# Kernel tuning notes

Hardware: AMD Instinct MI355X
Metric: run time of the kernel (lower is better)

The kernel has to match this reference:

```python
import jax, jax.numpy as jnp
import numpy as np

TEMPERATURE = 0.5
NEG_FILL = -9e15


def setup_inputs() -> dict:
    key = jax.random.key(0)
    k1, k2 = jax.random.split(key)
    B, D = 8192, 128
    z1 = jax.random.normal(k1, (B, D), dtype=jnp.float32)
    z2 = jax.random.normal(k2, (B, D), dtype=jnp.float32)
    return {"z1": z1, "z2": z2}


def reference(z1, z2):
    B = z1.shape[0]
    N = 2 * B
    z = jnp.concatenate([z1, z2], axis=0)              # [N, D]
    sim = jnp.matmul(z, z.T) / TEMPERATURE             # [N, N]
    eye = jnp.eye(N, dtype=bool)
    sim = jnp.where(eye, NEG_FILL, sim)
    idx = jnp.arange(N)
    pos_idx = (idx + B) % N
    positives = sim[idx, pos_idx]                      # [N]
    loss = -positives + jax.scipy.special.logsumexp(sim, axis=1)
    return loss.mean()
```

## Files before the change

kernel.cpp:

```cpp
#include <hip/hip_runtime.h>
#include <stdint.h>


typedef __attribute__((ext_vector_type(8))) short s16x8;
typedef __attribute__((ext_vector_type(16))) float f32x16;

#define N_TOT   16384
#define NHALF   8192
#define DDIM    128
#define NQ      16
#define QW      (N_TOT / NQ)
#define BN      64
#define NT      (QW / BN)
#define BM      256
#define NRB     (N_TOT / BM)
#define CSH     128.0f
#define LN2     0.69314718055994530942f
#define BF_SCALE 1.6986436f

__device__ __forceinline__ unsigned short f2bf(float f) {
    union { float f; unsigned int u; } v; v.f = f;
    unsigned int u = v.u;
    unsigned int r = (u + 0x7FFFu + ((u >> 16) & 1u)) >> 16;
    return (unsigned short)r;
}

__device__ __forceinline__ void gload_lds16(const void* g, void* l) {
    __builtin_amdgcn_global_load_lds(
        (const __attribute__((address_space(1))) void*)g,
        (__attribute__((address_space(3))) void*)l, 16, 0, 0);
}

__global__ __launch_bounds__(256) void k_castpos(const float* __restrict__ z1,
                                                 const float* __restrict__ z2,
                                                 unsigned short* __restrict__ zb,
                                                 float* __restrict__ pos_part,
                                                 float* __restrict__ ws_acc) {
    __shared__ float red[4];
    int i = blockIdx.x * 256 + threadIdx.x;
    if (i == 0) { ws_acc[0] = 0.f; ((unsigned int*)ws_acc)[1] = 0u; }
    float4 a = ((const float4*)z1)[i];
    float4 b = ((const float4*)z2)[i];
    ushort4 oa, ob;
    oa.x = f2bf(a.x * BF_SCALE); oa.y = f2bf(a.y * BF_SCALE);
    oa.z = f2bf(a.z * BF_SCALE); oa.w = f2bf(a.w * BF_SCALE);
    ob.x = f2bf(b.x * BF_SCALE); ob.y = f2bf(b.y * BF_SCALE);
    ob.z = f2bf(b.z * BF_SCALE); ob.w = f2bf(b.w * BF_SCALE);
    ((ushort4*)zb)[i] = oa;
    ((ushort4*)(zb + (size_t)NHALF * DDIM))[i] = ob;
    float s = a.x * b.x + a.y * b.y + a.z * b.z + a.w * b.w;
    for (int o = 32; o; o >>= 1) s += __shfl_xor(s, o);
    int lane = threadIdx.x & 63, w = threadIdx.x >> 6;
    if (lane == 0) red[w] = s;
    __syncthreads();
    if (threadIdx.x == 0) pos_part[blockIdx.x] = red[0] + red[1] + red[2] + red[3];
}

#define MFMA_SUB(TBASE, SDX, O0, O1) do {                                     \
    const int c_  = (SDX) * 32 + l31;                                         \
    const int cx_ = c_ & 15;                                                  \
    const s16x8* tb_ = (TBASE) + c_ * 16;                                     \
    O0 = acc_init; O1 = acc_init;                                             \
    _Pragma("unroll")                                                         \
    for (int ks_ = 0; ks_ < 8; ++ks_) {                                       \
        s16x8 a_ = tb_[(ks_ * 2 + h) ^ cx_];                                  \
        O0 = __builtin_amdgcn_mfma_f32_32x32x16_bf16(a_, rf0[ks_], O0, 0,0,0);\
        O1 = __builtin_amdgcn_mfma_f32_32x32x16_bf16(a_, rf1[ks_], O1, 0,0,0);\
    } } while (0)

#define EXP_SUB(X0, X1, CB) do {                                              \
    if ((CB) == rowB) {                                                       \
        _Pragma("unroll")                                                     \
        for (int r2_ = 0; r2_ < 16; ++r2_) {                                  \
            int crow_ = (r2_ & 3) + 8 * (r2_ >> 2) + 4 * h;                   \
            if (crow_ == l31) X0[r2_] = -1e30f;                               \
        } }                                                                   \
    if ((CB) == rowB + 32) {                                                  \
        _Pragma("unroll")                                                     \
        for (int r2_ = 0; r2_ < 16; ++r2_) {                                  \
            int crow_ = (r2_ & 3) + 8 * (r2_ >> 2) + 4 * h;                   \
            if (crow_ == l31) X1[r2_] = -1e30f;                               \
        } }                                                                   \
    _Pragma("unroll")                                                         \
    for (int r2_ = 0; r2_ < 16; r2_ += 4) {                                   \
        sa[0] += __builtin_amdgcn_exp2f(X0[r2_ + 0]);                         \
        sa[1] += __builtin_amdgcn_exp2f(X0[r2_ + 1]);                         \
        sa[2] += __builtin_amdgcn_exp2f(X0[r2_ + 2]);                         \
        sa[3] += __builtin_amdgcn_exp2f(X0[r2_ + 3]);                         \
        sb[0] += __builtin_amdgcn_exp2f(X1[r2_ + 0]);                         \
        sb[1] += __builtin_amdgcn_exp2f(X1[r2_ + 1]);                         \
        sb[2] += __builtin_amdgcn_exp2f(X1[r2_ + 2]);                         \
        sb[3] += __builtin_amdgcn_exp2f(X1[r2_ + 3]);                         \
    } } while (0)

__global__ __launch_bounds__(256) void k_main(const unsigned short* __restrict__ zb,
                                              float* __restrict__ ps) {
    __shared__ s16x8 tile[2][BN * 16];

    const int tid  = threadIdx.x;
    const int lane = tid & 63;
    const int w    = tid >> 6;
    const int h    = lane >> 5;
    const int l31  = lane & 31;

    const int bid = blockIdx.x;
    const int q   = bid >> 6;
    const int rb  = bid & 63;
    const int rowB     = rb * BM + w * 64;
    const int colStart = q * QW;

    s16x8 rf0[8], rf1[8];
    {
        const s16x8* rp0 = (const s16x8*)(zb + (size_t)(rowB + l31) * DDIM);
        const s16x8* rp1 = (const s16x8*)(zb + (size_t)(rowB + 32 + l31) * DDIM);
        #pragma unroll
        for (int ks = 0; ks < 8; ++ks) { rf0[ks] = rp0[ks * 2 + h]; rf1[ks] = rp1[ks * 2 + h]; }
    }

    int soff[4];
    #pragma unroll
    for (int j = 0; j < 4; ++j) {
        int e = w * 4 + j;
        int col = e * 4 + (lane >> 4);
        int chunk = (lane & 15) ^ (col & 15);
        soff[j] = col * 256 + chunk * 16;
    }

    #pragma unroll
    for (int j = 0; j < 4; ++j)
        gload_lds16((const char*)zb + (size_t)colStart * 256 + soff[j],
                    (char*)(&tile[0][0]) + (w * 4 + j) * 1024);
    #pragma unroll
    for (int j = 0; j < 4; ++j)
        gload_lds16((const char*)zb + (size_t)(colStart + BN) * 256 + soff[j],
                    (char*)(&tile[1][0]) + (w * 4 + j) * 1024);

    const f32x16 acc_init = {-CSH, -CSH, -CSH, -CSH, -CSH, -CSH, -CSH, -CSH,
                             -CSH, -CSH, -CSH, -CSH, -CSH, -CSH, -CSH, -CSH};
    float sa[4] = {0.f, 0.f, 0.f, 0.f};
    float sb[4] = {0.f, 0.f, 0.f, 0.f};
    f32x16 A0, A1, B0, B1;
    int pcb;

    asm volatile("s_waitcnt vmcnt(4)" ::: "memory");
    __builtin_amdgcn_s_barrier();
    {
        const s16x8* tbase = &tile[0][0];
        MFMA_SUB(tbase, 0, A0, A1);
        MFMA_SUB(tbase, 1, B0, B1);
        EXP_SUB(A0, A1, colStart);
        pcb = colStart + 32;
    }
    __builtin_amdgcn_s_barrier();
    #pragma unroll
    for (int j = 0; j < 4; ++j)
        gload_lds16((const char*)zb + (size_t)(colStart + 2 * BN) * 256 + soff[j],
                    (char*)(&tile[0][0]) + (w * 4 + j) * 1024);

    for (int t = 1; t < NT; ++t) {
        if (t < NT - 1) asm volatile("s_waitcnt vmcnt(4)" ::: "memory");
        else            asm volatile("s_waitcnt vmcnt(0)" ::: "memory");
        __builtin_amdgcn_s_barrier();
        const s16x8* tbase = &tile[0][0] + (t & 1) * (BN * 16);
        const int cb0 = colStart + t * BN;
        MFMA_SUB(tbase, 0, A0, A1);
        EXP_SUB(B0, B1, pcb);
        MFMA_SUB(tbase, 1, B0, B1);
        EXP_SUB(A0, A1, cb0);
        pcb = cb0 + 32;
        __builtin_amdgcn_s_barrier();
        if (t + 2 < NT) {
            #pragma unroll
            for (int j = 0; j < 4; ++j)
                gload_lds16((const char*)zb + (size_t)(colStart + (t + 2) * BN) * 256 + soff[j],
                            (char*)(&tile[0][0]) + (t & 1) * 16384 + (w * 4 + j) * 1024);
        }
    }
    EXP_SUB(B0, B1, pcb);

    float sA = (sa[0] + sa[1]) + (sa[2] + sa[3]);
    float sB = (sb[0] + sb[1]) + (sb[2] + sb[3]);
    sA += __shfl_xor(sA, 32);
    sB += __shfl_xor(sB, 32);
    if (lane < 32) {
        ps[(size_t)q * N_TOT + rowB + l31]      = sA;
        ps[(size_t)q * N_TOT + rowB + 32 + l31] = sB;
    }
}

__global__ __launch_bounds__(256) void k_cf(const float* __restrict__ ps,
                                            const float* __restrict__ pos_part,
                                            float* __restrict__ ws_acc,
                                            float* __restrict__ out) {
    __shared__ float red[4];
    __shared__ int last;
    const int tid = threadIdx.x;
    const int base = blockIdx.x * 1024;
    float ls = 0.f;
    #pragma unroll
    for (int k = 0; k < 4; ++k) {
        int row = base + k * 256 + tid;
        float s = 0.f;
        #pragma unroll
        for (int qq = 0; qq < NQ; ++qq) s += ps[(size_t)qq * N_TOT + row];
        ls += LN2 * (CSH + log2f(s));
    }
    for (int o = 32; o; o >>= 1) ls += __shfl_xor(ls, o);
    int lane = tid & 63, wv = tid >> 6;
    if (lane == 0) red[wv] = ls;
    __syncthreads();
    if (tid == 0) {
        atomicAdd(&ws_acc[0], red[0] + red[1] + red[2] + red[3]);
        __threadfence();
        unsigned int old = atomicAdd(&((unsigned int*)ws_acc)[1], 1u);
        last = (old == 15u) ? 1 : 0;
    }
    __syncthreads();
    if (last) {
        float p = pos_part[tid] + pos_part[tid + 256] +
                  pos_part[tid + 512] + pos_part[tid + 768];
        for (int o = 32; o; o >>= 1) p += __shfl_xor(p, o);
        if (lane == 0) red[wv] = p;
        __syncthreads();
        if (tid == 0) {
            float lse_tot = atomicAdd(&ws_acc[0], 0.f);
            float pos_tot = red[0] + red[1] + red[2] + red[3];
            out[0] = (lse_tot - 4.0f * pos_tot) * (1.0f / (float)N_TOT);
        }
    }
}

extern "C" void kernel_launch(void* const* d_in, const int* in_sizes, int n_in,
                              void* d_out, int out_size, void* d_ws, size_t ws_size,
                              hipStream_t stream) {
    const float* z1 = (const float*)d_in[0];
    const float* z2 = (const float*)d_in[1];
    float* out = (float*)d_out;

    char* ws = (char*)d_ws;
    float* ps       = (float*)ws;
    float* ws_acc   = (float*)(ws + (1u << 20));
    float* pos_part = (float*)(ws + (1u << 20) + 1024);
    unsigned short* zb = (unsigned short*)(ws + (2u << 20));

    k_castpos<<<dim3(1024), dim3(256), 0, stream>>>(z1, z2, zb, pos_part, ws_acc);
    k_main<<<dim3(NRB * NQ), dim3(256), 0, stream>>>(zb, ps);
    k_cf<<<dim3(16), dim3(256), 0, stream>>>(ps, pos_part, ws_acc, out);
}
```

Baseline: 134.9 us.

## Switch similarity GEMM to int8 MFMA with polynomial exp2 on packed FMA

Quantizes the embeddings to int8 with a fixed scale instead of bf16 and computes the similarity tiles with 32x32x32 i8 MFMA, halving the bytes staged through LDS and the matrix-instruction count. The hardware exp2 is replaced by a bit-trick exponent split plus a cubic polynomial evaluated with packed v_pk_fma_f32, spreading the transcendental work onto FMA pipes. The software pipeline that overlapped one sub-tile's exp with the next MFMA is dropped in favor of a simpler sequential loop. It risks accuracy from int8 quantization, clamping and the approximate exp, and may lose MFMA/VALU overlap.

```diff
diff --git a/kernel.cpp b/kernel.cpp
--- a/kernel.cpp
+++ b/kernel.cpp
@@ -2,12 +2,12 @@
 #include <stdint.h>
 
 
-typedef __attribute__((ext_vector_type(8))) short s16x8;
-typedef __attribute__((ext_vector_type(16))) float f32x16;
+typedef __attribute__((ext_vector_type(4)))  int   i32x4;
+typedef __attribute__((ext_vector_type(16))) int   i32x16;
+typedef __attribute__((ext_vector_type(2)))  float f32x2;
 
 #define N_TOT   16384
 #define NHALF   8192
-#define DDIM    128
 #define NQ      16
 #define QW      (N_TOT / NQ)
 #define BN      64
@@ -16,14 +16,7 @@
 #define NRB     (N_TOT / BM)
 #define CSH     128.0f
 #define LN2     0.69314718055994530942f
-#define BF_SCALE 1.6986436f
-
-__device__ __forceinline__ unsigned short f2bf(float f) {
-    union { float f; unsigned int u; } v; v.f = f;
-    unsigned int u = v.u;
-    unsigned int r = (u + 0x7FFFu + ((u >> 16) & 1u)) >> 16;
-    return (unsigned short)r;
-}
+#define QS      27.178299f
 
 __device__ __forceinline__ void gload_lds16(const void* g, void* l) {
     __builtin_amdgcn_global_load_lds(
@@ -31,9 +24,24 @@
         (__attribute__((address_space(3))) void*)l, 16, 0, 0);
 }
 
+__device__ __forceinline__ f32x2 pk_fma(f32x2 a, f32x2 b, f32x2 c) {
+    f32x2 d;
+    asm("v_pk_fma_f32 %0, %1, %2, %3" : "=v"(d) : "v"(a), "v"(b), "v"(c));
+    return d;
+}
+
+__device__ __forceinline__ unsigned pack4(float4 f) {
+    int q0 = (int)rintf(fminf(fmaxf(f.x * QS, -127.f), 127.f));
+    int q1 = (int)rintf(fminf(fmaxf(f.y * QS, -127.f), 127.f));
+    int q2 = (int)rintf(fminf(fmaxf(f.z * QS, -127.f), 127.f));
+    int q3 = (int)rintf(fminf(fmaxf(f.w * QS, -127.f), 127.f));
+    return (unsigned)(q0 & 255) | ((unsigned)(q1 & 255) << 8) |
+           ((unsigned)(q2 & 255) << 16) | ((unsigned)q3 << 24);
+}
+
 __global__ __launch_bounds__(256) void k_castpos(const float* __restrict__ z1,
                                                  const float* __restrict__ z2,
-                                                 unsigned short* __restrict__ zb,
+                                                 unsigned* __restrict__ zb,
                                                  float* __restrict__ pos_part,
                                                  float* __restrict__ ws_acc) {
     __shared__ float red[4];
@@ -41,13 +49,8 @@
     if (i == 0) { ws_acc[0] = 0.f; ((unsigned int*)ws_acc)[1] = 0u; }
     float4 a = ((const float4*)z1)[i];
     float4 b = ((const float4*)z2)[i];
-    ushort4 oa, ob;
-    oa.x = f2bf(a.x * BF_SCALE); oa.y = f2bf(a.y * BF_SCALE);
-    oa.z = f2bf(a.z * BF_SCALE); oa.w = f2bf(a.w * BF_SCALE);
-    ob.x = f2bf(b.x * BF_SCALE); ob.y = f2bf(b.y * BF_SCALE);
-    ob.z = f2bf(b.z * BF_SCALE); ob.w = f2bf(b.w * BF_SCALE);
-    ((ushort4*)zb)[i] = oa;
-    ((ushort4*)(zb + (size_t)NHALF * DDIM))[i] = ob;
+    zb[i]          = pack4(a);
+    zb[i + 262144] = pack4(b);
     float s = a.x * b.x + a.y * b.y + a.z * b.z + a.w * b.w;
     for (int o = 32; o; o >>= 1) s += __shfl_xor(s, o);
     int lane = threadIdx.x & 63, w = threadIdx.x >> 6;
@@ -56,46 +59,55 @@
     if (threadIdx.x == 0) pos_part[blockIdx.x] = red[0] + red[1] + red[2] + red[3];
 }
 
-#define MFMA_SUB(TBASE, SDX, O0, O1) do {                                     \
-    const int c_  = (SDX) * 32 + l31;                                         \
-    const int cx_ = c_ & 15;                                                  \
-    const s16x8* tb_ = (TBASE) + c_ * 16;                                     \
-    O0 = acc_init; O1 = acc_init;                                             \
+#define MFMA_SUB(TB, SDX, O0, O1) do {                                        \
+    const int c_ = (SDX) * 32 + l31;                                          \
+    O0 = kZ16; O1 = kZ16;                                                     \
     _Pragma("unroll")                                                         \
-    for (int ks_ = 0; ks_ < 8; ++ks_) {                                       \
-        s16x8 a_ = tb_[(ks_ * 2 + h) ^ cx_];                                  \
-        O0 = __builtin_amdgcn_mfma_f32_32x32x16_bf16(a_, rf0[ks_], O0, 0,0,0);\
-        O1 = __builtin_amdgcn_mfma_f32_32x32x16_bf16(a_, rf1[ks_], O1, 0,0,0);\
+    for (int m_ = 0; m_ < 4; ++m_) {                                          \
+        i32x4 a_ = *(const i32x4*)((TB) + (m_ * 2 + h) * 1024 + c_ * 16);     \
+        O0 = __builtin_amdgcn_mfma_i32_32x32x32_i8(a_, rf0[m_], O0, 0, 0, 0); \
+        O1 = __builtin_amdgcn_mfma_i32_32x32x32_i8(a_, rf1[m_], O1, 0, 0, 0); \
     } } while (0)
+
+#define EXP_PAIR(AI0, AI1, S0, S1) do {                                       \
+    int i0_ = (AI0); i0_ = i0_ < 512 ? 512 : i0_;                             \
+    int i1_ = (AI1); i1_ = i1_ < 512 ? 512 : i1_;                             \
+    f32x2 af_; af_[0] = (float)i0_; af_[1] = (float)i1_;                      \
+    f32x2 T_ = pk_fma(af_, kD2, kMG);                                         \
+    f32x2 Nn_ = pk_fma(T_, kM1, kMG);                                         \
+    f32x2 F_ = pk_fma(af_, kD2, Nn_);                                         \
+    f32x2 P_ = pk_fma(F_, kC3, kC2);                                          \
+    P_ = pk_fma(F_, P_, kC1);                                                 \
+    P_ = pk_fma(F_, P_, kC0);                                                 \
+    unsigned n0_ = __float_as_uint(T_[0]) - 0x4B0000C0u;                      \
+    unsigned n1_ = __float_as_uint(T_[1]) - 0x4B0000C0u;                      \
+    S0 += __uint_as_float((n0_ << 23) + __float_as_uint(P_[0]));              \
+    S1 += __uint_as_float((n1_ << 23) + __float_as_uint(P_[1]));              \
+} while (0)
 
 #define EXP_SUB(X0, X1, CB) do {                                              \
     if ((CB) == rowB) {                                                       \
         _Pragma("unroll")                                                     \
         for (int r2_ = 0; r2_ < 16; ++r2_) {                                  \
             int crow_ = (r2_ & 3) + 8 * (r2_ >> 2) + 4 * h;                   \
-            if (crow_ == l31) X0[r2_] = -1e30f;                               \
+            if (crow_ == l31) X0[r2_] = -(1 << 30);                           \
         } }                                                                   \
     if ((CB) == rowB + 32) {                                                  \
         _Pragma("unroll")                                                     \
         for (int r2_ = 0; r2_ < 16; ++r2_) {                                  \
             int crow_ = (r2_ & 3) + 8 * (r2_ >> 2) + 4 * h;                   \
-            if (crow_ == l31) X1[r2_] = -1e30f;                               \
+            if (crow_ == l31) X1[r2_] = -(1 << 30);                           \
         } }                                                                   \
     _Pragma("unroll")                                                         \
-    for (int r2_ = 0; r2_ < 16; r2_ += 4) {                                   \
-        sa[0] += __builtin_amdgcn_exp2f(X0[r2_ + 0]);                         \
-        sa[1] += __builtin_amdgcn_exp2f(X0[r2_ + 1]);                         \
-        sa[2] += __builtin_amdgcn_exp2f(X0[r2_ + 2]);                         \
-        sa[3] += __builtin_amdgcn_exp2f(X0[r2_ + 3]);                         \
-        sb[0] += __builtin_amdgcn_exp2f(X1[r2_ + 0]);                         \
-        sb[1] += __builtin_amdgcn_exp2f(X1[r2_ + 1]);                         \
-        sb[2] += __builtin_amdgcn_exp2f(X1[r2_ + 2]);                         \
-        sb[3] += __builtin_amdgcn_exp2f(X1[r2_ + 3]);                         \
+    for (int p_ = 0; p_ < 8; ++p_) {                                          \
+        EXP_PAIR(X0[2 * p_], X0[2 * p_ + 1], sa[p_ & 3], sa[(p_ + 2) & 3]);   \
+        EXP_PAIR(X1[2 * p_], X1[2 * p_ + 1], sb[p_ & 3], sb[(p_ + 2) & 3]);   \
     } } while (0)
 
-__global__ __launch_bounds__(256) void k_main(const unsigned short* __restrict__ zb,
+__global__ __launch_bounds__(256) void k_main(const unsigned* __restrict__ zbu,
                                               float* __restrict__ ps) {
-    __shared__ s16x8 tile[2][BN * 16];
+    __shared__ char tile[2][8192];
+    const char* zb8 = (const char*)zbu;
 
     const int tid  = threadIdx.x;
     const int lane = tid & 63;
@@ -109,74 +121,57 @@
     const int rowB     = rb * BM + w * 64;
     const int colStart = q * QW;
 
-    s16x8 rf0[8], rf1[8];
-    {
-        const s16x8* rp0 = (const s16x8*)(zb + (size_t)(rowB + l31) * DDIM);
-        const s16x8* rp1 = (const s16x8*)(zb + (size_t)(rowB + 32 + l31) * DDIM);
-        #pragma unroll
-        for (int ks = 0; ks < 8; ++ks) { rf0[ks] = rp0[ks * 2 + h]; rf1[ks] = rp1[ks * 2 + h]; }
-    }
-
-    int soff[4];
-    #pragma unroll
-    for (int j = 0; j < 4; ++j) {
-        int e = w * 4 + j;
-        int col = e * 4 + (lane >> 4);
-        int chunk = (lane & 15) ^ (col & 15);
-        soff[j] = col * 256 + chunk * 16;
-    }
-
-    #pragma unroll
-    for (int j = 0; j < 4; ++j)
-        gload_lds16((const char*)zb + (size_t)colStart * 256 + soff[j],
-                    (char*)(&tile[0][0]) + (w * 4 + j) * 1024);
-    #pragma unroll
-    for (int j = 0; j < 4; ++j)
-        gload_lds16((const char*)zb + (size_t)(colStart + BN) * 256 + soff[j],
-                    (char*)(&tile[1][0]) + (w * 4 + j) * 1024);
-
-    const f32x16 acc_init = {-CSH, -CSH, -CSH, -CSH, -CSH, -CSH, -CSH, -CSH,
-                             -CSH, -CSH, -CSH, -CSH, -CSH, -CSH, -CSH, -CSH};
+    i32x4 rf0[4], rf1[4];
+    #pragma unroll
+    for (int m = 0; m < 4; ++m) {
+        rf0[m] = *(const i32x4*)(zb8 + (size_t)(rowB + l31) * 128 + m * 32 + h * 16);
+        rf1[m] = *(const i32x4*)(zb8 + (size_t)(rowB + 32 + l31) * 128 + m * 32 + h * 16);
+    }
+
+    int gsoff[2];
+    #pragma unroll
+    for (int j = 0; j < 2; ++j) gsoff[j] = lane * 128 + (w * 2 + j) * 16;
+
+    #pragma unroll
+    for (int j = 0; j < 2; ++j)
+        gload_lds16(zb8 + (size_t)colStart * 128 + gsoff[j],
+                    &tile[0][0] + (w * 2 + j) * 1024);
+    #pragma unroll
+    for (int j = 0; j < 2; ++j)
+        gload_lds16(zb8 + (size_t)(colStart + BN) * 128 + gsoff[j],
+                    &tile[1][0] + (w * 2 + j) * 1024);
+
+    const i32x16 kZ16 = {};
+    const f32x2 kD2 = {0.00390625f, 0.00390625f};
+    const f32x2 kMG = {8388672.0f, 8388672.0f};
+    const f32x2 kM1 = {-1.0f, -1.0f};
+    const f32x2 kC3 = {0.05550411f, 0.05550411f};
+    const f32x2 kC2 = {0.24022651f, 0.24022651f};
+    const f32x2 kC1 = {0.69314718f, 0.69314718f};
+    const f32x2 kC0 = {1.0f, 1.0f};
+
     float sa[4] = {0.f, 0.f, 0.f, 0.f};
     float sb[4] = {0.f, 0.f, 0.f, 0.f};
-    f32x16 A0, A1, B0, B1;
-    int pcb;
-
-    asm volatile("s_waitcnt vmcnt(4)" ::: "memory");
-    __builtin_amdgcn_s_barrier();
-    {
-        const s16x8* tbase = &tile[0][0];
-        MFMA_SUB(tbase, 0, A0, A1);
-        MFMA_SUB(tbase, 1, B0, B1);
-        EXP_SUB(A0, A1, colStart);
-        pcb = colStart + 32;
-    }
-    __builtin_amdgcn_s_barrier();
-    #pragma unroll
-    for (int j = 0; j < 4; ++j)
-        gload_lds16((const char*)zb + (size_t)(colStart + 2 * BN) * 256 + soff[j],
-                    (char*)(&tile[0][0]) + (w * 4 + j) * 1024);
-
-    for (int t = 1; t < NT; ++t) {
-        if (t < NT - 1) asm volatile("s_waitcnt vmcnt(4)" ::: "memory");
+    i32x16 A0, A1;
+
+    for (int t = 0; t < NT; ++t) {
+        if (t < NT - 1) asm volatile("s_waitcnt vmcnt(2)" ::: "memory");
         else            asm volatile("s_waitcnt vmcnt(0)" ::: "memory");
         __builtin_amdgcn_s_barrier();
-        const s16x8* tbase = &tile[0][0] + (t & 1) * (BN * 16);
+        const char* tb = &tile[t & 1][0];
         const int cb0 = colStart + t * BN;
-        MFMA_SUB(tbase, 0, A0, A1);
-        EXP_SUB(B0, B1, pcb);
-        MFMA_SUB(tbase, 1, B0, B1);
+        MFMA_SUB(tb, 0, A0, A1);
         EXP_SUB(A0, A1, cb0);
-        pcb = cb0 + 32;
+        MFMA_SUB(tb, 1, A0, A1);
+        EXP_SUB(A0, A1, cb0 + 32);
         __builtin_amdgcn_s_barrier();
         if (t + 2 < NT) {
             #pragma unroll
-            for (int j = 0; j < 4; ++j)
-                gload_lds16((const char*)zb + (size_t)(colStart + (t + 2) * BN) * 256 + soff[j],
-                            (char*)(&tile[0][0]) + (t & 1) * 16384 + (w * 4 + j) * 1024);
+            for (int j = 0; j < 2; ++j)
+                gload_lds16(zb8 + (size_t)(colStart + (t + 2) * BN) * 128 + gsoff[j],
+                            &tile[t & 1][0] + (w * 2 + j) * 1024);
         }
     }
-    EXP_SUB(B0, B1, pcb);
 
     float sA = (sa[0] + sa[1]) + (sa[2] + sa[3]);
     float sB = (sb[0] + sb[1]) + (sb[2] + sb[3]);
@@ -241,7 +236,7 @@
     float* ps       = (float*)ws;
     float* ws_acc   = (float*)(ws + (1u << 20));
     float* pos_part = (float*)(ws + (1u << 20) + 1024);
-    unsigned short* zb = (unsigned short*)(ws + (2u << 20));
+    unsigned* zb    = (unsigned*)(ws + (2u << 20));
 
     k_castpos<<<dim3(1024), dim3(256), 0, stream>>>(z1, z2, zb, pos_part, ws_acc);
     k_main<<<dim3(NRB * NQ), dim3(256), 0, stream>>>(zb, ps);
```

Result: slower. 155.4 us (+15.2%).
